# Kernel optimization log

Measured on AMD Instinct MI355X. Metric: run time of the kernel, lower is better.

Reference implementation:

```python
import jax, jax.numpy as jnp
import numpy as np

B, T, C = 2, 1024, 1024
H = 16
HS = C // H          # head size = 64
ROT = HS // 2        # partial rotary dims = 32
CTX = 1024           # ctx_len (T <= CTX)
FFN_H = 3 * 1024     # GeGLU hidden = 3 * n_ffn
LN_EPS = 1e-5


def setup_inputs():
    key = jax.random.key(0)
    ks = jax.random.split(key, 20)
    s = 0.02
    f32 = jnp.float32
    p = {}
    p["x"] = jax.random.normal(ks[0], (B, T, C), f32)
    p["ln1_w"] = jnp.ones((C,), f32); p["ln1_b"] = jnp.zeros((C,), f32)
    p["ln2_w"] = jnp.ones((C,), f32); p["ln2_b"] = jnp.zeros((C,), f32)
    p["Wq"] = jax.random.normal(ks[1], (C, C), f32) * s; p["bq"] = jnp.zeros((C,), f32)
    p["Wk"] = jax.random.normal(ks[2], (C, C), f32) * s; p["bk"] = jnp.zeros((C,), f32)
    p["Wv"] = jax.random.normal(ks[3], (C, C), f32) * s; p["bv"] = jnp.zeros((C,), f32)
    p["Wo"] = jax.random.normal(ks[4], (C, C), f32) * s; p["bo"] = jnp.zeros((C,), f32)
    p["time_w"] = 1.0 + 0.01 * jax.random.normal(ks[5], (H, CTX), f32)
    p["time_alpha"] = 1.0 + 0.01 * jax.random.normal(ks[6], (H, 1, CTX), f32)
    p["time_beta"] = 1.0 + 0.01 * jax.random.normal(ks[7], (H, CTX, 1), f32)
    p["time_gamma"] = 1.0 + 0.01 * jax.random.normal(ks[8], (CTX, 1), f32)
    p["mix_w"] = jnp.eye(H, dtype=f32) + 0.02 * jax.random.normal(ks[9], (H, H), f32)
    p["Wkg"] = jax.random.normal(ks[10], (C, FFN_H), f32) * s; p["bkg"] = jnp.zeros((FFN_H,), f32)
    p["Wvg"] = jax.random.normal(ks[11], (C, FFN_H), f32) * s; p["bvg"] = jnp.zeros((FFN_H,), f32)
    p["Wwg"] = jax.random.normal(ks[12], (FFN_H, C), f32) * s; p["bwg"] = jnp.zeros((C,), f32)
    return p


def _ln(x, w, b):
    m = jnp.mean(x, axis=-1, keepdims=True)
    v = jnp.mean((x - m) ** 2, axis=-1, keepdims=True)
    return (x - m) * jax.lax.rsqrt(v + LN_EPS) * w + b


def _time_shift_half(x):
    # ZeroPad2d((0,0,1,-1)) on the first C//2 channels: shift down by one step in time
    c = x.shape[-1]
    shifted = jnp.pad(x[:, :-1, : c // 2], ((0, 0), (1, 0), (0, 0)))
    return jnp.concatenate([shifted, x[:, :, c // 2 :]], axis=-1)


def _decay_w(time_w, time_alpha, time_beta):
    # Toeplitz trick: [H, CTX] -> circulant [H, CTX, CTX] of relative-time weights
    TT = CTX
    w = jnp.pad(time_w, ((0, 0), (0, TT)))                 # [H, 2TT]
    w = jnp.tile(w, (1, TT))[:, :-TT]                      # [H, 2TT*TT - TT]
    w = w.reshape(-1, TT, 2 * TT - 1)[:, :, TT - 1 :]      # [H, TT, TT]
    return w[:, :T, :T] * time_alpha[:, :, :T] * time_beta[:, :T, :]


def _rotate_half(x):
    x1, x2 = x[..., : x.shape[-1] // 2], x[..., x.shape[-1] // 2 :]
    return jnp.concatenate([-x2, x1], axis=-1)


def _apply_rotary(q, k):
    # q, k: [B, H, T, ROT]
    inv_freq = 1.0 / (10000.0 ** (jnp.arange(0, ROT, 2, dtype=jnp.float32) / ROT))
    t = jnp.arange(T, dtype=jnp.float32)
    freqs = t[:, None] * inv_freq[None, :]                 # [T, ROT//2]
    emb = jnp.concatenate([freqs, freqs], axis=-1)         # [T, ROT]
    cos, sin = jnp.cos(emb), jnp.sin(emb)
    q = q * cos + _rotate_half(q) * sin
    k = k * cos + _rotate_half(k) * sin
    return q, k


def _mha_pro(x, Wq, bq, Wk, bk, Wv, bv, Wo, bo,
             time_w, time_alpha, time_beta, time_gamma, mix_w):
    w = _decay_w(time_w, time_alpha, time_beta)            # [H, T, T]
    xs = _time_shift_half(x)
    q = (xs @ Wq + bq).reshape(B, T, H, HS).transpose(0, 2, 1, 3)
    k = (xs @ Wk + bk).reshape(B, T, H, HS).transpose(0, 2, 1, 3)
    v = (xs @ Wv + bv).reshape(B, T, H, HS).transpose(0, 2, 1, 3)
    qr, qp = q[..., :ROT], q[..., ROT:]
    kr, kp = k[..., :ROT], k[..., ROT:]
    qr, kr = _apply_rotary(qr, kr)
    q = jnp.concatenate([qr, qp], axis=-1)
    k = jnp.concatenate([kr, kp], axis=-1)
    att = jnp.einsum('bhqd,bhkd->bhqk', q, k) * (1.0 / np.sqrt(HS))
    causal = jnp.tril(jnp.ones((T, T), dtype=bool))
    att = jnp.where(causal, att, -jnp.inf)
    att = jax.nn.softmax(att, axis=-1)
    att = att * w                                          # learned time-decay reweighting
    att = jnp.einsum('oi,biqk->boqk', mix_w, att)          # 1x1 conv head mixing
    y = jnp.einsum('bhqk,bhkd->bhqd', att, v)
    y = y.transpose(0, 2, 1, 3).reshape(B, T, C)
    return (y @ Wo + bo) * time_gamma[:T, :]


def _geglu(x, Wkg, bkg, Wvg, bvg, Wwg, bwg):
    kk = x @ Wkg + bkg
    vv = x @ Wvg + bvg
    return (jax.nn.gelu(kk, approximate=False) * vv) @ Wwg + bwg


def _block(x, ln1_w, ln1_b, ln2_w, ln2_b, Wq, bq, Wk, bk, Wv, bv, Wo, bo,
           time_w, time_alpha, time_beta, time_gamma, mix_w,
           Wkg, bkg, Wvg, bvg, Wwg, bwg):
    x = x + _mha_pro(_ln(x, ln1_w, ln1_b), Wq, bq, Wk, bk, Wv, bv, Wo, bo,
                     time_w, time_alpha, time_beta, time_gamma, mix_w)
    x = x + _geglu(_ln(x, ln2_w, ln2_b), Wkg, bkg, Wvg, bvg, Wwg, bwg)
    return x


def reference(x, ln1_w, ln1_b, ln2_w, ln2_b, Wq, bq, Wk, bk, Wv, bv, Wo, bo,
              time_w, time_alpha, time_beta, time_gamma, mix_w,
              Wkg, bkg, Wvg, bvg, Wwg, bwg):
    return _block(x, ln1_w, ln1_b, ln2_w, ln2_b, Wq, bq, Wk, bk, Wv, bv, Wo, bo,
                  time_w, time_alpha, time_beta, time_gamma, mix_w,
                  Wkg, bkg, Wvg, bvg, Wwg, bwg)
```

## Files before the change

### kernel.cpp

```cpp
#include <hip/hip_runtime.h>
#include <cstdint>
#include <cstddef>
#include <cstdio>

#define B_   2
#define T_   1024
#define C_   1024
#define H_   16
#define HS_  64
#define FFN_ 3072

typedef __bf16   bf16x8 __attribute__((ext_vector_type(8)));
typedef float    f32x4  __attribute__((ext_vector_type(4)));
typedef float    f32x16 __attribute__((ext_vector_type(16)));
typedef uint16_t u16x8  __attribute__((ext_vector_type(8)));

__device__ __forceinline__ uint16_t f2bf(float f){
  uint32_t u = __float_as_uint(f);
  u += 0x7FFFu + ((u >> 16) & 1u);
  return (uint16_t)(u >> 16);
}
__device__ __forceinline__ float bf2f(uint16_t h){
  return __uint_as_float(((uint32_t)h) << 16);
}
__device__ __forceinline__ bf16x8 ldb8(const uint16_t* p){
  return __builtin_bit_cast(bf16x8, *reinterpret_cast<const u16x8*>(p));
}
__device__ __forceinline__ f32x4 mfma16(bf16x8 a, bf16x8 b, f32x4 c){
  return __builtin_amdgcn_mfma_f32_16x16x32_bf16(a, b, c, 0, 0, 0);
}

typedef __attribute__((address_space(1))) const uint32_t* gas_t;
typedef __attribute__((address_space(3))) uint32_t* las_t;
__device__ __forceinline__ void gl_lds16(const uint16_t* g, uint16_t* l){
  __builtin_amdgcn_global_load_lds((gas_t)g, (las_t)l, 16, 0, 0);
}

__global__ __launch_bounds__(256) void k_prep(
    const float* __restrict__ Wq, const float* __restrict__ Wk,
    const float* __restrict__ Wv, const float* __restrict__ Wo,
    const float* __restrict__ Wkg, const float* __restrict__ Wvg,
    const float* __restrict__ Wwg,
    const float* __restrict__ bq, const float* __restrict__ bk,
    const float* __restrict__ bv, const float* __restrict__ bkg,
    const float* __restrict__ bvg,
    const float* __restrict__ x, const float* __restrict__ ln1w,
    const float* __restrict__ ln1b,
    uint16_t* __restrict__ WqT, uint16_t* __restrict__ WkT,
    uint16_t* __restrict__ WvT, uint16_t* __restrict__ WoT,
    uint16_t* __restrict__ Wff, uint16_t* __restrict__ WwgT,
    float* __restrict__ bcat, float* __restrict__ bcatFF,
    uint16_t* __restrict__ xs)
{
  __shared__ float tile[32][33];
  __shared__ float red[8];
  const int id = blockIdx.x;
  const int tid = threadIdx.x;

  if (id < 13312){
    if (id < 4096){
      int w = id >> 10, r = id & 1023;
      const float* in = (w==0)?Wq:(w==1)?Wk:(w==2)?Wv:Wo;
      uint16_t* outp  = (w==0)?WqT:(w==1)?WkT:(w==2)?WvT:WoT;
      int c0 = (r & 31)*32, r0 = (r >> 5)*32;
      int tx = tid & 31, ty = tid >> 5;
      #pragma unroll
      for (int i=0;i<4;i++) tile[ty+i*8][tx] = in[(size_t)(r0+ty+i*8)*1024 + c0+tx];
      __syncthreads();
      #pragma unroll
      for (int i=0;i<4;i++) outp[(size_t)(c0+ty+i*8)*1024 + r0+tx] = f2bf(tile[tx][ty+i*8]);
    } else if (id < 10240){
      int r = id - 4096; int s = r / 3072; r -= s*3072;
      const float* in = s ? Wvg : Wkg;
      int c0 = (r % 96)*32, r0 = (r / 96)*32;
      int tx = tid & 31, ty = tid >> 5;
      #pragma unroll
      for (int i=0;i<4;i++) tile[ty+i*8][tx] = in[(size_t)(r0+ty+i*8)*3072 + c0+tx];
      __syncthreads();
      #pragma unroll
      for (int i=0;i<4;i++){
        int j = c0+ty+i*8;
        int row = ((j>>4)<<5) + (s<<4) + (j&15);
        Wff[(size_t)row*1024 + r0+tx] = f2bf(tile[tx][ty+i*8]);
      }
    } else {
      int r = id - 10240;
      int c0 = (r & 31)*32, r0 = (r >> 5)*32;
      int tx = tid & 31, ty = tid >> 5;
      #pragma unroll
      for (int i=0;i<4;i++) tile[ty+i*8][tx] = Wwg[(size_t)(r0+ty+i*8)*1024 + c0+tx];
      __syncthreads();
      #pragma unroll
      for (int i=0;i<4;i++) WwgT[(size_t)(c0+ty+i*8)*3072 + r0+tx] = f2bf(tile[tx][ty+i*8]);
    }
    return;
  }
  if (id < 13324){
    int i = (id - 13312)*256 + tid;
    float v;
    if      (i < 1024) v = bq[i];
    else if (i < 2048) v = bk[i-1024];
    else               v = bv[i-2048];
    bcat[i] = v;
    return;
  }
  if (id < 13348){
    int i = (id - 13324)*256 + tid;
    int s = (i >> 4) & 1;
    int j = ((i >> 5) << 4) | (i & 15);
    bcatFF[i] = s ? bvg[j] : bkg[j];
    return;
  }
  {
    int row = id - 13348;
    int t = row & (T_-1);
    const float* xr = x + (size_t)row*C_;
    float4 v = reinterpret_cast<const float4*>(xr)[tid];
    float s  = v.x+v.y+v.z+v.w;
    float s2 = v.x*v.x+v.y*v.y+v.z*v.z+v.w*v.w;
    #pragma unroll
    for (int o=1;o<64;o<<=1){ s += __shfl_xor(s,o); s2 += __shfl_xor(s2,o); }
    int lane = tid & 63, wv = tid >> 6;
    if (lane == 0){ red[wv] = s; red[4+wv] = s2; }
    __syncthreads();
    s  = red[0]+red[1]+red[2]+red[3];
    s2 = red[4]+red[5]+red[6]+red[7];
    float mean = s * (1.f/1024.f);
    float var  = s2 * (1.f/1024.f) - mean*mean;
    float rs   = rsqrtf(var + 1e-5f);
    float vals[4] = {v.x, v.y, v.z, v.w};
    #pragma unroll
    for (int j=0;j<4;j++){
      int cc = tid*4 + j;
      float o_ = (vals[j]-mean)*rs*ln1w[cc] + ln1b[cc];
      uint16_t ob = f2bf(o_);
      if (cc < 512){
        if (t < T_-1) xs[(size_t)(row+1)*C_ + cc] = ob;
        if (t == 0)   xs[(size_t)row*C_ + cc] = 0;
      } else {
        xs[(size_t)row*C_ + cc] = ob;
      }
    }
  }
}

__global__ __launch_bounds__(256) void k_ln(const float* __restrict__ in,
                                            const float* __restrict__ w,
                                            const float* __restrict__ bia,
                                            uint16_t* __restrict__ out){
  int row = blockIdx.x;
  const float* xr = in + (size_t)row*C_;
  float4 v = reinterpret_cast<const float4*>(xr)[threadIdx.x];
  float s  = v.x+v.y+v.z+v.w;
  float s2 = v.x*v.x+v.y*v.y+v.z*v.z+v.w*v.w;
  #pragma unroll
  for (int o=1;o<64;o<<=1){ s += __shfl_xor(s,o); s2 += __shfl_xor(s2,o); }
  __shared__ float red[8];
  int lane = threadIdx.x & 63, wid = threadIdx.x >> 6;
  if (lane == 0){ red[wid] = s; red[4+wid] = s2; }
  __syncthreads();
  s  = red[0]+red[1]+red[2]+red[3];
  s2 = red[4]+red[5]+red[6]+red[7];
  float mean = s * (1.f/1024.f);
  float var  = s2 * (1.f/1024.f) - mean*mean;
  float rs   = rsqrtf(var + 1e-5f);
  float vals[4] = {v.x, v.y, v.z, v.w};
  #pragma unroll
  for (int j=0;j<4;j++){
    int cc = threadIdx.x*4 + j;
    out[(size_t)row*C_ + cc] = f2bf((vals[j]-mean)*rs*w[cc] + bia[cc]);
  }
}

enum { EPI_QKV=0, EPI_WO=2, EPI_GEGLU=3, EPI_FFN2=4 };

template<int EPI, int BN>
__global__ __launch_bounds__(256) void k_gemm2(
    const uint16_t* __restrict__ A, const uint16_t* __restrict__ Bt,
    const float* __restrict__ bias, void* __restrict__ outp,
    int M, int N, int K,
    const float* __restrict__ aux0, const float* __restrict__ aux1)
{
  __shared__ uint16_t As[128*64];
  __shared__ uint16_t Bs[BN*64];
  const int m0 = blockIdx.y*128, n0 = blockIdx.x*BN;
  const int tid = threadIdx.x;
  const int lane = tid & 63, wid = tid >> 6;
  const int wy = wid >> 1, wx = wid & 1;
  const int l16 = lane & 15, lr = lane >> 4;
  const int sw = l16 & 7;
  const int WN = BN/2;
  const int NW = BN/32;
  const f32x4 z = {0.f,0.f,0.f,0.f};
  f32x4 acc[4][NW];
  #pragma unroll
  for (int m=0;m<4;m++)
    #pragma unroll
    for (int n=0;n<NW;n++) acc[m][n] = z;

  for (int k0 = 0; k0 < K; k0 += 64){
    #pragma unroll
    for (int r4=0;r4<4;r4++){
      int c = tid + r4*256;
      int row = c >> 3, jp = c & 7;
      int col = ((jp ^ (row & 7)) << 3);
      gl_lds16(A + (size_t)(m0+row)*K + k0 + col, As + c*8);
    }
    #pragma unroll
    for (int r4=0;r4<BN/32;r4++){
      int c = tid + r4*256;
      int row = c >> 3, jp = c & 7;
      int col = ((jp ^ (row & 7)) << 3);
      gl_lds16(Bt + (size_t)(n0+row)*K + k0 + col, Bs + c*8);
    }
    __syncthreads();
    #pragma unroll
    for (int kk=0;kk<2;kk++){
      bf16x8 af[4], bfr[NW];
      #pragma unroll
      for (int m=0;m<4;m++)
        af[m] = ldb8(As + (wy*64 + m*16 + l16)*64 + (((lr + 4*kk) ^ sw) << 3));
      #pragma unroll
      for (int n=0;n<NW;n++)
        bfr[n] = ldb8(Bs + (wx*WN + n*16 + l16)*64 + (((lr + 4*kk) ^ sw) << 3));
      #pragma unroll
      for (int m=0;m<4;m++)
        #pragma unroll
        for (int n=0;n<NW;n++) acc[m][n] = mfma16(af[m], bfr[n], acc[m][n]);
    }
    __syncthreads();
  }
  if constexpr (EPI == EPI_QKV){
    const float linvf = exp2f(-(float)l16 * 0.83048202f);
    #pragma unroll
    for (int m=0;m<4;m++){
      #pragma unroll
      for (int r=0;r<4;r++){
        int row = m0 + wy*64 + m*16 + lr*4 + r;
        int bb = row >> 10, t = row & 1023;
        int col0 = n0 + wx*32 + l16;
        float v0 = acc[m][0][r] + bias[col0];
        float v1 = acc[m][1][r] + bias[col0+16];
        int kind = col0 >> 10, hcol = col0 & 1023;
        int h = hcol >> 6, d0 = hcol & 63;
        if (kind < 2 && wx == 0){
          float sn, cs;
          __sincosf((float)t * linvf, &sn, &cs);
          float r0 = v0*cs - v1*sn;
          float r1 = v1*cs + v0*sn;
          v0 = r0; v1 = r1;
        }
        uint16_t* dst = (uint16_t*)outp + (size_t)kind*2097152;
        if (kind < 2){
          size_t basei = (((size_t)bb*16 + h)*1024 + t)*64;
          dst[basei + d0]      = f2bf(v0);
          dst[basei + d0 + 16] = f2bf(v1);
        } else {
          size_t basei = ((size_t)bb*16 + h)*65536;
          dst[basei + (size_t)d0*1024 + t]      = f2bf(v0);
          dst[basei + (size_t)(d0+16)*1024 + t] = f2bf(v1);
        }
      }
    }
  } else if constexpr (EPI == EPI_GEGLU){
    const int colb = n0 + wx*WN;
    #pragma unroll
    for (int m=0;m<4;m++){
      #pragma unroll
      for (int r=0;r<4;r++){
        int row = m0 + wy*64 + m*16 + lr*4 + r;
        #pragma unroll
        for (int np=0;np<NW;np+=2){
          float kk = acc[m][np][r]   + bias[colb + np*16 + l16];
          float vv = acc[m][np+1][r] + bias[colb + (np+1)*16 + l16];
          float gl = 0.5f*kk*(1.f + erff(kk*0.70710678118f));
          int j = ((colb>>5) + (np>>1))*16 + l16;
          ((uint16_t*)outp)[(size_t)row*3072 + j] = f2bf(gl*vv);
        }
      }
    }
  } else {
    #pragma unroll
    for (int m=0;m<4;m++){
      #pragma unroll
      for (int n=0;n<NW;n++){
        int col = n0 + wx*WN + n*16 + l16;
        float bc_ = bias ? bias[col] : 0.f;
        #pragma unroll
        for (int r=0;r<4;r++){
          int row = m0 + wy*64 + m*16 + lr*4 + r;
          float v = acc[m][n][r] + bc_;
          if constexpr (EPI == EPI_WO){
            int t = row & (T_-1);
            ((float*)outp)[(size_t)row*N + col] = aux1[(size_t)row*N + col] + v*aux0[t];
          } else {
            ((float*)outp)[(size_t)row*N + col] = aux0[(size_t)row*N + col] + v;
          }
        }
      }
    }
  }
}

__global__ __launch_bounds__(256) void k_stats(const uint16_t* __restrict__ q,
                                               const uint16_t* __restrict__ kmat,
                                               float* __restrict__ sm, float* __restrict__ sl){
  int bh = blockIdx.x, qb = blockIdx.y;
  int lane = threadIdx.x & 63, wid = threadIdx.x >> 6;
  int l16 = lane & 15, lr = lane >> 4;
  int r0 = qb*64 + wid*16;
  const uint16_t* qh = q    + (size_t)bh*T_*HS_;
  const uint16_t* kh = kmat + (size_t)bh*T_*HS_;
  int kq = lr*8;
  bf16x8 a0 = ldb8(qh + (size_t)(r0 + l16)*HS_ + kq);
  bf16x8 a1 = ldb8(qh + (size_t)(r0 + l16)*HS_ + kq + 32);
  float m_[4], l_[4]; int rows[4];
  #pragma unroll
  for (int r=0;r<4;r++){ m_[r] = -1e30f; l_[r] = 0.f; rows[r] = r0 + lr*4 + r; }
  int ktmax = (r0 + 15) >> 4;
  for (int kt = 0; kt <= ktmax; kt++){
    bf16x8 b0 = ldb8(kh + (size_t)(kt*16 + l16)*HS_ + kq);
    bf16x8 b1 = ldb8(kh + (size_t)(kt*16 + l16)*HS_ + kq + 32);
    f32x4 s = {0.f,0.f,0.f,0.f};
    s = mfma16(a0, b0, s);
    s = mfma16(a1, b1, s);
    int kcol = kt*16 + l16;
    #pragma unroll
    for (int r=0;r<4;r++){
      float sv = (kcol <= rows[r]) ? s[r]*0.125f : -3.0e38f;
      float mn = fmaxf(m_[r], sv);
      l_[r] = l_[r]*__expf(m_[r] - mn) + __expf(sv - mn);
      m_[r] = mn;
    }
  }
  #pragma unroll
  for (int o=1;o<16;o<<=1){
    #pragma unroll
    for (int r=0;r<4;r++){
      float mo = __shfl_xor(m_[r], o);
      float lo = __shfl_xor(l_[r], o);
      float mn = fmaxf(m_[r], mo);
      l_[r] = l_[r]*__expf(m_[r] - mn) + lo*__expf(mo - mn);
      m_[r] = mn;
    }
  }
  if (l16 == 0){
    #pragma unroll
    for (int r=0;r<4;r++){
      sm[(size_t)bh*T_ + rows[r]] = m_[r];
      sl[(size_t)bh*T_ + rows[r]] = l_[r];
    }
  }
}

__global__ __launch_bounds__(512, 2) void k_attn(
    const uint16_t* __restrict__ q, const uint16_t* __restrict__ kmat,
    const uint16_t* __restrict__ vT,
    const float* __restrict__ sm, const float* __restrict__ sl,
    const float* __restrict__ tw, const float* __restrict__ alpha,
    const float* __restrict__ beta, const float* __restrict__ mixw,
    uint16_t* __restrict__ py, int* __restrict__ counter)
{
  __shared__ uint32_t U32[2*4096];
  __shared__ uint16_t Cm[2*8320];
  __shared__ uint16_t TWL[16*160];
  __shared__ int s_item;

  const int tid = threadIdx.x;
  const int lane = tid & 63;
  const int wid = __builtin_amdgcn_readfirstlane(tid >> 6);
  const int l16 = lane & 15, lr = lane >> 4;
  const int l32 = lane & 31, g32 = lane >> 5;

  bf16x8 mwf;
  {
    u16x8 t8;
    #pragma unroll
    for (int j=0;j<8;j++){
      float v = (l32 < 16) ? mixw[l32*16 + g32*8 + j] : 0.f;
      t8[j] = f2bf(v);
    }
    mwf = __builtin_bit_cast(bf16x8, t8);
  }
  const f32x4 z = {0.f,0.f,0.f,0.f};

  for (;;){
    if (tid == 0) s_item = atomicAdd(counter, 1);
    __syncthreads();
    const int item = s_item;
    if (item >= 576) break;

    const int b = (item >= 288) ? 1 : 0;
    int j = item - b*288;
    int g = 0;
    while (4*(g+1)*(g+2) <= j) g++;
    int jj = j - 4*g*(g+1);
    const int qt = 8*g + jj/(g+1);
    const int kc = jj % (g+1);

    const int q0 = qt*16, ck0 = kc*128;
    const int lc = min(127, q0 + 15 - ck0);
    const int nt = (lc >> 5) + 1;

    const int base = 1008 - q0 + ck0;
    for (int i = tid; i < 16*144; i += 512){
      int h = i / 144, t = i - h*144;
      int gi = base + t;
      TWL[h*160 + t] = (gi <= 1023) ? f2bf(tw[h*1024 + gi]) : (uint16_t)0;
    }
    float SM[2][4], BSL[2][4];
    bf16x8 qa[2][2];
    #pragma unroll
    for (int h2=0; h2<2; ++h2){
      int h = 2*wid + h2, bh = b*16 + h;
      float4 s4 = *reinterpret_cast<const float4*>(sm   + (size_t)bh*1024 + q0 + lr*4);
      float4 l4 = *reinterpret_cast<const float4*>(sl   + (size_t)bh*1024 + q0 + lr*4);
      float4 b4 = *reinterpret_cast<const float4*>(beta + (size_t)h*1024  + q0 + lr*4);
      SM[h2][0]=s4.x; SM[h2][1]=s4.y; SM[h2][2]=s4.z; SM[h2][3]=s4.w;
      BSL[h2][0]=b4.x/l4.x; BSL[h2][1]=b4.y/l4.y; BSL[h2][2]=b4.z/l4.z; BSL[h2][3]=b4.w/l4.w;
      #pragma unroll
      for (int kk=0;kk<2;kk++)
        qa[h2][kk] = ldb8(q + ((size_t)bh*1024 + q0 + l16)*64 + kk*32 + lr*8);
    }
    f32x4 acc[2][4];
    #pragma unroll
    for (int oo=0;oo<2;oo++) for (int n=0;n<4;n++) acc[oo][n] = z;

    __syncthreads();

    for (int tp = 0; tp < nt; tp += 2){
      const int ntile = (nt - tp >= 2) ? 2 : 1;
      bf16x8 vf[2][2][4];
      #pragma unroll
      for (int half = 0; half < 2; ++half){
        if (half >= ntile) break;
        const int t = tp + half;
        const int k0 = ck0 + t*32;
        #pragma unroll
        for (int oo=0;oo<2;oo++){
          const uint16_t* vh = vT + (size_t)(b*16 + 2*wid + oo)*65536;
          #pragma unroll
          for (int n=0;n<4;n++)
            vf[half][oo][n] = ldb8(vh + (size_t)(n*16 + l16)*1024 + k0 + lr*8);
        }
        float al0[2], al1[2];
        #pragma unroll
        for (int n=0;n<2;n++){
          int kg = k0 + n*16 + l16;
          al0[n] = alpha[(2*wid+0)*1024 + kg];
          al1[n] = alpha[(2*wid+1)*1024 + kg];
        }
        f32x4 s[2][2];
        s[0][0]=z; s[0][1]=z; s[1][0]=z; s[1][1]=z;
        #pragma unroll
        for (int h2=0;h2<2;h2++){
          const uint16_t* kh = kmat + ((size_t)(b*16 + 2*wid + h2)*1024 + k0)*64;
          #pragma unroll
          for (int kk=0;kk<2;kk++){
            bf16x8 kb0 = ldb8(kh + (size_t)(l16)*64      + kk*32 + lr*8);
            bf16x8 kb1 = ldb8(kh + (size_t)(16 + l16)*64 + kk*32 + lr*8);
            s[h2][0] = mfma16(qa[h2][kk], kb0, s[h2][0]);
            s[h2][1] = mfma16(qa[h2][kk], kb1, s[h2][1]);
          }
        }
        uint32_t* Ub = U32 + half*4096;
        #pragma unroll
        for (int n=0;n<2;n++){
          int kloc = n*16 + l16;
          int kg = k0 + kloc;
          #pragma unroll
          for (int r=0;r<4;r++){
            int qloc = lr*4 + r;
            bool ok = (kg <= q0 + qloc);
            int twi = 15 - qloc + (kg - ck0);
            float u0 = 0.f, u1 = 0.f;
            if (ok){
              u0 = __expf(s[0][n][r]*0.125f - SM[0][r]) * BSL[0][r] * al0[n] * bf2f(TWL[(2*wid+0)*160 + twi]);
              u1 = __expf(s[1][n][r]*0.125f - SM[1][r]) * BSL[1][r] * al1[n] * bf2f(TWL[(2*wid+1)*160 + twi]);
            }
            uint32_t pk = (uint32_t)f2bf(u0) | ((uint32_t)f2bf(u1) << 16);
            Ub[wid*512 + qloc*32 + ((kloc + 8*(qloc>>2)) & 31)] = pk;
          }
        }
      }
      __syncthreads();
      #pragma unroll
      for (int half = 0; half < 2; ++half){
        if (half >= ntile) break;
        const uint32_t* Ub = U32 + half*4096;
        uint16_t* Cb = Cm + half*8320;
        #pragma unroll
        for (int cc=0; cc<2; ++cc){
          int qrow = wid*2 + cc;
          int pbase = qrow*32;
          int swz = (l32 + 8*(qrow>>2)) & 31;
          u16x8 a8;
          uint32_t* a32 = reinterpret_cast<uint32_t*>(&a8);
          #pragma unroll
          for (int jv=0;jv<4;jv++)
            a32[jv] = Ub[(4*g32 + jv)*512 + pbase + swz];
          bf16x8 a = __builtin_bit_cast(bf16x8, a8);
          f32x16 zz{};
          __builtin_amdgcn_s_setprio(1);
          f32x16 dd = __builtin_amdgcn_mfma_f32_32x32x16_bf16(a, mwf, zz, 0, 0, 0);
          __builtin_amdgcn_s_setprio(0);
          if (l32 < 16){
            int o = l32;
            #pragma unroll
            for (int rg=0; rg<4; ++rg){
              int p0 = pbase + rg*8 + g32*4;
              uint32_t w0 = (uint32_t)f2bf(dd[4*rg+0]) | ((uint32_t)f2bf(dd[4*rg+1]) << 16);
              uint32_t w1 = (uint32_t)f2bf(dd[4*rg+2]) | ((uint32_t)f2bf(dd[4*rg+3]) << 16);
              uint2 pk2; pk2.x = w0; pk2.y = w1;
              *reinterpret_cast<uint2*>(Cb + (size_t)o*520 + p0) = pk2;
            }
          }
        }
      }
      __syncthreads();
      #pragma unroll
      for (int half = 0; half < 2; ++half){
        if (half >= ntile) break;
        const uint16_t* Cb = Cm + half*8320;
        #pragma unroll
        for (int oo=0;oo<2;oo++){
          int o = 2*wid + oo;
          bf16x8 cf = ldb8(Cb + (size_t)o*520 + l16*32 + lr*8);
          __builtin_amdgcn_s_setprio(1);
          #pragma unroll
          for (int n=0;n<4;n++)
            acc[oo][n] = mfma16(cf, vf[half][oo][n], acc[oo][n]);
          __builtin_amdgcn_s_setprio(0);
        }
      }
    }

    uint16_t* po = py + (((size_t)(b*64 + qt))*8 + kc)*16384;
    #pragma unroll
    for (int oo=0;oo<2;oo++){
      int o = 2*wid + oo;
      #pragma unroll
      for (int n=0;n<4;n++)
        #pragma unroll
        for (int r=0;r<4;r++){
          int qloc = lr*4 + r;
          po[o*1024 + qloc*64 + n*16 + l16] = f2bf(acc[oo][n][r]);
        }
    }
    __syncthreads();
  }
}

__global__ void k_yred(const uint16_t* __restrict__ py, uint16_t* __restrict__ y){
  int idx = blockIdx.x*256 + threadIdx.x;
  int d8 = idx & 7, qq = (idx>>3)&15, o = (idx>>7)&15, qt = (idx>>11)&63, b = idx>>17;
  int nch = (qt>>3) + 1;
  const uint16_t* p0 = py + (((size_t)(b*64+qt))*8)*16384 + o*1024 + qq*64 + d8*8;
  float s[8] = {0,0,0,0,0,0,0,0};
  for (int kc=0; kc<nch; kc++){
    u16x8 v = *reinterpret_cast<const u16x8*>(p0 + (size_t)kc*16384);
    #pragma unroll
    for (int e=0;e<8;e++) s[e] += bf2f(v[e]);
  }
  int t = qt*16 + qq;
  u16x8 w;
  #pragma unroll
  for (int e=0;e<8;e++) w[e] = f2bf(s[e]);
  *reinterpret_cast<u16x8*>(y + ((size_t)(b*1024 + t))*1024 + o*64 + d8*8) = w;
}

extern "C" void kernel_launch(void* const* d_in, const int* in_sizes, int n_in,
                              void* d_out, int out_size, void* d_ws, size_t ws_size,
                              hipStream_t stream)
{
  const float* x      = (const float*)d_in[0];
  const float* ln1w   = (const float*)d_in[1];
  const float* ln1b   = (const float*)d_in[2];
  const float* ln2w   = (const float*)d_in[3];
  const float* ln2b   = (const float*)d_in[4];
  const float* Wq     = (const float*)d_in[5];
  const float* bq     = (const float*)d_in[6];
  const float* Wk     = (const float*)d_in[7];
  const float* bk     = (const float*)d_in[8];
  const float* Wv     = (const float*)d_in[9];
  const float* bv     = (const float*)d_in[10];
  const float* Wo     = (const float*)d_in[11];
  const float* bo     = (const float*)d_in[12];
  const float* tw     = (const float*)d_in[13];
  const float* talpha = (const float*)d_in[14];
  const float* tbeta  = (const float*)d_in[15];
  const float* tgamma = (const float*)d_in[16];
  const float* mixw   = (const float*)d_in[17];
  const float* Wkg    = (const float*)d_in[18];
  const float* bkg    = (const float*)d_in[19];
  const float* Wvg    = (const float*)d_in[20];
  const float* bvg    = (const float*)d_in[21];
  const float* Wwg    = (const float*)d_in[22];
  const float* bwg    = (const float*)d_in[23];

  char* ws = (char*)d_ws;
  size_t off = 0;
  auto alloc = [&](size_t bytes)->char*{
    char* p = ws + off; off += (bytes + 255) & ~(size_t)255; return p;
  };
  int*      counter = (int*)alloc(256);
  uint16_t* WqT  = (uint16_t*)alloc((size_t)C_*C_*2);
  uint16_t* WkT  = (uint16_t*)alloc((size_t)C_*C_*2);
  uint16_t* WvT  = (uint16_t*)alloc((size_t)C_*C_*2);
  uint16_t* WoT  = (uint16_t*)alloc((size_t)C_*C_*2);
  uint16_t* Wff  = (uint16_t*)alloc((size_t)2*FFN_*C_*2);
  uint16_t* WwgT = (uint16_t*)alloc((size_t)C_*FFN_*2);
  uint16_t* xs   = (uint16_t*)alloc((size_t)B_*T_*C_*2);
  uint16_t* qbuf = (uint16_t*)alloc((size_t)B_*T_*C_*2);
  uint16_t* kbuf = (uint16_t*)alloc((size_t)B_*T_*C_*2);
  uint16_t* vT   = (uint16_t*)alloc((size_t)B_*T_*C_*2);
  float*    sm   = (float*)alloc((size_t)B_*H_*T_*4);
  float*    sl   = (float*)alloc((size_t)B_*H_*T_*4);
  uint16_t* ybuf = (uint16_t*)alloc((size_t)B_*T_*C_*2);
  float*    x1   = (float*)alloc((size_t)B_*T_*C_*4);
  float*    bcat   = (float*)alloc((size_t)3072*4);
  float*    bcatFF = (float*)alloc((size_t)6144*4);
  char*     region = alloc((size_t)33*1024*1024);
  uint16_t* py  = (uint16_t*)region;
  uint16_t* gb  = (uint16_t*)region;

  if (off > ws_size){
    fprintf(stderr, "kernel_launch: ws too small (%zu needed, %zu given)\n", off, ws_size);
    return;
  }

  hipMemsetAsync(counter, 0, 4, stream);

  dim3 blk(256);
  k_prep<<<15396, blk, 0, stream>>>(Wq, Wk, Wv, Wo, Wkg, Wvg, Wwg,
                                    bq, bk, bv, bkg, bvg,
                                    x, ln1w, ln1b,
                                    WqT, WkT, WvT, WoT, Wff, WwgT,
                                    bcat, bcatFF, xs);

  k_gemm2<EPI_QKV,64><<<dim3(48,16), blk, 0, stream>>>(xs, WqT, bcat, qbuf, 2048, 3072, 1024, nullptr, nullptr);

  k_stats<<<dim3(B_*H_, T_/64), blk, 0, stream>>>(qbuf, kbuf, sm, sl);
  k_attn<<<dim3(512), dim3(512), 0, stream>>>(qbuf, kbuf, vT, sm, sl,
                                              tw, talpha, tbeta, mixw, py, counter);
  k_yred<<<1024, blk, 0, stream>>>(py, ybuf);

  k_gemm2<EPI_WO,64><<<dim3(16,16), blk, 0, stream>>>(ybuf, WoT, bo, x1, 2048, 1024, 1024, tgamma, x);

  k_ln<<<B_*T_, blk, 0, stream>>>(x1, ln2w, ln2b, xs);

  k_gemm2<EPI_GEGLU,128><<<dim3(48,16), blk, 0, stream>>>(xs, Wff, bcatFF, gb, 2048, 6144, 1024, nullptr, nullptr);
  k_gemm2<EPI_FFN2,64><<<dim3(16,16), blk, 0, stream>>>(gb, WwgT, bwg, d_out, 2048, 1024, 3072, x1, nullptr);
}
```

Baseline: 250.6 us.

## Widen QKV GEMM tile and prefetch K fragments in attention loop

New measurement: 266.2 us. 6.2% more time.

```diff
diff --git a/kernel.cpp b/kernel.cpp
--- a/kernel.cpp
+++ b/kernel.cpp
@@ -231,6 +231,9 @@
     __syncthreads();
   }
   if constexpr (EPI == EPI_QKV){
+    const int colb = n0 + wx*WN;
+    const int kind = colb >> 10;
+    const int h = (colb >> 6) & 15;
     const float linvf = exp2f(-(float)l16 * 0.83048202f);
     #pragma unroll
     for (int m=0;m<4;m++){
@@ -238,27 +241,24 @@
       for (int r=0;r<4;r++){
         int row = m0 + wy*64 + m*16 + lr*4 + r;
         int bb = row >> 10, t = row & 1023;
-        int col0 = n0 + wx*32 + l16;
-        float v0 = acc[m][0][r] + bias[col0];
-        float v1 = acc[m][1][r] + bias[col0+16];
-        int kind = col0 >> 10, hcol = col0 & 1023;
-        int h = hcol >> 6, d0 = hcol & 63;
-        if (kind < 2 && wx == 0){
+        float v[NW];
+        #pragma unroll
+        for (int n=0;n<NW;n++) v[n] = acc[m][n][r] + bias[colb + n*16 + l16];
+        if (kind < 2){
           float sn, cs;
           __sincosf((float)t * linvf, &sn, &cs);
-          float r0 = v0*cs - v1*sn;
-          float r1 = v1*cs + v0*sn;
-          v0 = r0; v1 = r1;
-        }
-        uint16_t* dst = (uint16_t*)outp + (size_t)kind*2097152;
-        if (kind < 2){
+          float r0 = v[0]*cs - v[1]*sn;
+          float r1 = v[1]*cs + v[0]*sn;
+          v[0] = r0; v[1] = r1;
+          uint16_t* dst = (uint16_t*)outp + (size_t)kind*2097152;
           size_t basei = (((size_t)bb*16 + h)*1024 + t)*64;
-          dst[basei + d0]      = f2bf(v0);
-          dst[basei + d0 + 16] = f2bf(v1);
+          #pragma unroll
+          for (int n=0;n<NW;n++) dst[basei + n*16 + l16] = f2bf(v[n]);
         } else {
+          uint16_t* dst = (uint16_t*)outp + (size_t)2*2097152;
           size_t basei = ((size_t)bb*16 + h)*65536;
-          dst[basei + (size_t)d0*1024 + t]      = f2bf(v0);
-          dst[basei + (size_t)(d0+16)*1024 + t] = f2bf(v1);
+          #pragma unroll
+          for (int n=0;n<NW;n++) dst[basei + (size_t)(n*16 + l16)*1024 + t] = f2bf(v[n]);
         }
       }
     }
@@ -426,6 +426,26 @@
     #pragma unroll
     for (int oo=0;oo<2;oo++) for (int n=0;n<4;n++) acc[oo][n] = z;
 
+    bf16x8 kf[2][2][2][2];
+    {
+      const int nt0 = (nt >= 2) ? 2 : 1;
+      #pragma unroll
+      for (int half = 0; half < 2; ++half){
+        if (half < nt0){
+          const int k0 = ck0 + half*32;
+          #pragma unroll
+          for (int h2=0;h2<2;h2++){
+            const uint16_t* kh = kmat + ((size_t)(b*16 + 2*wid + h2)*1024 + k0)*64;
+            #pragma unroll
+            for (int kk=0;kk<2;kk++){
+              kf[half][h2][kk][0] = ldb8(kh + (size_t)(l16)*64      + kk*32 + lr*8);
+              kf[half][h2][kk][1] = ldb8(kh + (size_t)(16 + l16)*64 + kk*32 + lr*8);
+            }
+          }
+        }
+      }
+    }
+
     __syncthreads();
 
     for (int tp = 0; tp < nt; tp += 2){
@@ -454,13 +474,10 @@
         s[0][0]=z; s[0][1]=z; s[1][0]=z; s[1][1]=z;
         #pragma unroll
         for (int h2=0;h2<2;h2++){
-          const uint16_t* kh = kmat + ((size_t)(b*16 + 2*wid + h2)*1024 + k0)*64;
           #pragma unroll
           for (int kk=0;kk<2;kk++){
-            bf16x8 kb0 = ldb8(kh + (size_t)(l16)*64      + kk*32 + lr*8);
-            bf16x8 kb1 = ldb8(kh + (size_t)(16 + l16)*64 + kk*32 + lr*8);
-            s[h2][0] = mfma16(qa[h2][kk], kb0, s[h2][0]);
-            s[h2][1] = mfma16(qa[h2][kk], kb1, s[h2][1]);
+            s[h2][0] = mfma16(qa[h2][kk], kf[half][h2][kk][0], s[h2][0]);
+            s[h2][1] = mfma16(qa[h2][kk], kf[half][h2][kk][1], s[h2][1]);
           }
         }
         uint32_t* Ub = U32 + half*4096;
@@ -484,6 +501,24 @@
         }
       }
       __syncthreads();
+      {
+        const int tpn = tp + 2;
+        #pragma unroll
+        for (int half = 0; half < 2; ++half){
+          if (tpn + half < nt){
+            const int k0 = ck0 + (tpn + half)*32;
+            #pragma unroll
+            for (int h2=0;h2<2;h2++){
+              const uint16_t* kh = kmat + ((size_t)(b*16 + 2*wid + h2)*1024 + k0)*64;
+              #pragma unroll
+              for (int kk=0;kk<2;kk++){
+                kf[half][h2][kk][0] = ldb8(kh + (size_t)(l16)*64      + kk*32 + lr*8);
+                kf[half][h2][kk][1] = ldb8(kh + (size_t)(16 + l16)*64 + kk*32 + lr*8);
+              }
+            }
+          }
+        }
+      }
       #pragma unroll
       for (int half = 0; half < 2; ++half){
         if (half >= ntile) break;
@@ -638,7 +673,7 @@
                                     WqT, WkT, WvT, WoT, Wff, WwgT,
                                     bcat, bcatFF, xs);
 
-  k_gemm2<EPI_QKV,64><<<dim3(48,16), blk, 0, stream>>>(xs, WqT, bcat, qbuf, 2048, 3072, 1024, nullptr, nullptr);
+  k_gemm2<EPI_QKV,128><<<dim3(24,16), blk, 0, stream>>>(xs, WqT, bcat, qbuf, 2048, 3072, 1024, nullptr, nullptr);
 
   k_stats<<<dim3(B_*H_, T_/64), blk, 0, stream>>>(qbuf, kbuf, sm, sl);
   k_attn<<<dim3(512), dim3(512), 0, stream>>>(qbuf, kbuf, vT, sm, sl,
```
